# Kernel tuning notes

Measured on AMD Instinct MI355X. Metric: run time of the kernel, lower is better.

## Reference

```python
import jax, jax.numpy as jnp
import numpy as np

N_NODES = 10000
N_EDGES = 160000
MUL = 16          # multiplicity (num_radial channels) per irrep
EMB = 64          # radial_embed_size
HID = 128         # radial_hidden_size
N_PATHS = 5       # (0,0,0),(1,1,0),(0,1,1),(1,0,1),(1,1,1)
W_NUMEL = N_PATHS * MUL * MUL  # 1280


def setup_inputs() -> dict:
    key = jax.random.key(0)
    ks = jax.random.split(key, 9)
    return {
        'edge_index': jax.random.randint(ks[0], (2, N_EDGES), 0, N_NODES),
        'node_feat': jax.random.normal(ks[1], (N_NODES, 4 * MUL), dtype=jnp.float32),
        'edge_feat': jax.random.normal(ks[2], (N_EDGES, 4), dtype=jnp.float32),
        'edge_embed': jax.random.normal(ks[3], (N_EDGES, EMB), dtype=jnp.float32),
        'fc_w1': jax.random.normal(ks[4], (EMB, HID), dtype=jnp.float32),
        'fc_w2': jax.random.normal(ks[5], (HID, HID), dtype=jnp.float32),
        'fc_w3': jax.random.normal(ks[6], (HID, W_NUMEL), dtype=jnp.float32),
        'sc_w0': jax.random.normal(ks[7], (MUL, MUL), dtype=jnp.float32),
        'sc_w1': jax.random.normal(ks[8], (MUL, MUL), dtype=jnp.float32),
    }


def reference(edge_index, node_feat, edge_feat, edge_embed,
              fc_w1, fc_w2, fc_w3, sc_w0, sc_w1):
    """InfGCN GCNLayer: gather src features, fully-connected e3nn-style tensor
    product (irreps '16x0e+16x1o' x SH '1x0e+1x1o' -> '16x0e+16x1o') with
    per-edge weights from a radial MLP, scatter-add into dst, plus o3.Linear
    self-connection. e3nn conventions: FullyConnectedNet normalizes each layer
    by 1/sqrt(fan_in), component irrep_normalization gives w3j factors 1/sqrt(3)
    (1x1->0 dot) and 1/sqrt(2) (1x1->1 cross), element path_normalization gives
    per-path 1/sqrt(mul_in)."""
    E = edge_embed.shape[0]
    N = node_feat.shape[0]
    src, dst = edge_index[0], edge_index[1]

    # radial network (silu on hidden layers, e3nn fan-in normalization)
    h = jax.nn.silu(edge_embed @ (fc_w1 / np.sqrt(EMB)))
    h = jax.nn.silu(h @ (fc_w2 / np.sqrt(HID)))
    w = (h @ (fc_w3 / np.sqrt(HID))).reshape(E, N_PATHS, MUL, MUL)  # [E,P,u,w]

    # gather + split src features into l=0 / l=1 parts
    x = node_feat[src]                       # [E, 64]
    x0 = x[:, :MUL]                          # [E, u]
    x1 = x[:, MUL:].reshape(E, MUL, 3)       # [E, u, 3]
    y0 = edge_feat[:, :1]                    # [E, 1]
    y1 = edge_feat[:, 1:4]                   # [E, 3]

    inv = 1.0 / np.sqrt(MUL)                 # path fan-in normalization
    # l=0 output: paths (0,0,0) and (1,1,0)
    dot = jnp.einsum('eud,ed->eu', x1, y1) / np.sqrt(3.0)
    o0 = (jnp.einsum('euw,eu->ew', w[:, 0], x0 * y0)
          + jnp.einsum('euw,eu->ew', w[:, 1], dot)) * inv     # [E, w]
    # l=1 output: paths (0,1,1), (1,0,1), (1,1,1)
    cross = jnp.cross(x1, y1[:, None, :]) / np.sqrt(2.0)       # [E, u, 3]
    o1 = (jnp.einsum('euw,eu,ed->ewd', w[:, 2], x0, y1)
          + jnp.einsum('euw,eud->ewd', w[:, 3], x1 * y0[:, :, None])
          + jnp.einsum('euw,eud->ewd', w[:, 4], cross)) * inv  # [E, w, 3]

    msg = jnp.concatenate([o0, o1.reshape(E, 3 * MUL)], axis=-1)  # [E, 64]
    out = jax.ops.segment_sum(msg, dst, num_segments=N)            # [N, 64]

    # self-connection: o3.Linear, per-l channel mixing
    s0 = (node_feat[:, :MUL] @ sc_w0) * inv
    s1 = jnp.einsum('nud,uw->nwd', node_feat[:, MUL:].reshape(N, MUL, 3), sc_w1) * inv
    return out + jnp.concatenate([s0, s1.reshape(N, 3 * MUL)], axis=-1)
```

## Files before the change

kernel.cpp:

```cpp
#include <hip/hip_runtime.h>

#define NNODES 10000
#define NEDGES 160000
#define MUL 16
#define EMB 64
#define HID 128

#define RS128 0.08838834764831845f
#define SC3   (0.08838834764831845f * 0.25f)

typedef __attribute__((ext_vector_type(8))) _Float16 half8;
typedef __attribute__((ext_vector_type(4))) _Float16 half4;
typedef __attribute__((ext_vector_type(4))) float f32x4;

__global__ __launch_bounds__(256) void selfconn_kernel(
    const float* __restrict__ node_feat,
    const float* __restrict__ sc_w0,
    const float* __restrict__ sc_w1,
    float* __restrict__ out)
{
    const int tid = threadIdx.x;
    const int nl = tid >> 4;
    const int wp = tid & 15;
    const int n  = blockIdx.x * 16 + nl;

    __shared__ float nf[16][64];
    __shared__ float w0s[16][16];
    __shared__ float w1s[16][16];

    ((float4*)nf)[tid] = ((const float4*)(node_feat + (size_t)blockIdx.x * 16 * 64))[tid];
    if (tid < 64)       ((float4*)w0s)[tid]      = ((const float4*)sc_w0)[tid];
    else if (tid < 128) ((float4*)w1s)[tid - 64] = ((const float4*)sc_w1)[tid - 64];
    __syncthreads();

    float o0 = 0.f, o1x = 0.f, o1y = 0.f, o1z = 0.f;
#pragma unroll
    for (int u = 0; u < 16; ++u) {
        o0 += nf[nl][u] * w0s[u][wp];
        const float wv = w1s[u][wp];
        o1x += nf[nl][16 + u * 3 + 0] * wv;
        o1y += nf[nl][16 + u * 3 + 1] * wv;
        o1z += nf[nl][16 + u * 3 + 2] * wv;
    }
    float* op = out + (size_t)n * 64;
    op[wp]              = o0  * 0.25f;
    op[16 + wp * 3 + 0] = o1x * 0.25f;
    op[16 + wp * 3 + 1] = o1y * 0.25f;
    op[16 + wp * 3 + 2] = o1z * 0.25f;
}

__global__ __launch_bounds__(256) void prep_kernel(
    const float* __restrict__ w1,
    const float* __restrict__ w2,
    const float* __restrict__ w3,
    _Float16* __restrict__ wp)
{
    int idx = blockIdx.x * 256 + threadIdx.x;
    if (idx < 8192) {
        int j = idx & 7, lane = (idx >> 3) & 63, ks = (idx >> 9) & 1, nt = idx >> 10;
        int k = ks * 32 + (lane >> 4) * 8 + j;
        int n = nt * 16 + (lane & 15);
        wp[idx] = (_Float16)(w1[k * HID + n] * 0.125f);
    } else if (idx < 24576) {
        int t = idx - 8192;
        int j = t & 7, lane = (t >> 3) & 63, ks = (t >> 9) & 3, nt = t >> 11;
        int k = ks * 32 + (lane >> 4) * 8 + j;
        int n = nt * 16 + (lane & 15);
        wp[idx] = (_Float16)(w2[k * HID + n] * RS128);
    } else if (idx < 188416) {
        int t = idx - 24576;
        int j = t & 7, lane = (t >> 3) & 63, ks = (t >> 9) & 3, nt = t >> 11;
        int k = ks * 32 + (lane >> 4) * 8 + j;
        int n = nt * 16 + (lane & 15);
        wp[idx] = (_Float16)(w3[k * 1280 + n] * SC3);
    }
}

#define EE_OFF   0
#define H1_OFF   4096
#define H2_OFF   12288
#define SA_OFF   20480
#define SB_OFF   22528
#define SX_OFF   24576
#define SP3_OFF  26624
#define SP4_OFF  32768
#define SY_OFF   38912
#define SEF_OFF  39296
#define SIDX_OFF 39808
#define SMEM_BYTES 40064
#define OPW 65

__global__ __launch_bounds__(256, 4) void edge_mfma_kernel(
    const int*   __restrict__ ei,
    const float* __restrict__ node_feat,
    const float* __restrict__ edge_feat,
    const float* __restrict__ edge_embed,
    const _Float16* __restrict__ wpk,
    float* __restrict__ out)
{
    __shared__ __align__(16) char smem[SMEM_BYTES];

    const int tid = threadIdx.x;
    const int e0  = blockIdx.x * 32;

    int*   sidxp = (int*)(smem + SIDX_OFF);
    float* sEFp  = (float*)(smem + SEF_OFF);

    if (tid < 32)       sidxp[tid] = ei[e0 + tid];
    else if (tid < 64)  sidxp[tid] = ei[NEDGES + e0 + (tid - 32)];
    else if (tid < 192) {
        int t = tid - 64;
        sEFp[t] = edge_feat[e0 * 4 + t];
    }
    __syncthreads();

    float* xg = (float*)(smem + H1_OFF);
    {
        const float4* eesrc = (const float4*)(edge_embed + (size_t)e0 * EMB);
#pragma unroll
        for (int it = 0; it < 2; ++it) {
            int f = tid + it * 256;
            int row = f >> 4, c4 = f & 15;
            float4 v = eesrc[f];
            half4 h = { (_Float16)v.x, (_Float16)v.y, (_Float16)v.z, (_Float16)v.w };
            *(half4*)(smem + EE_OFF + row * 128 + ((c4 * 8) ^ ((row & 7) << 4))) = h;

            int src = sidxp[row];
            float4 nv = ((const float4*)(node_feat + (size_t)src * 64))[c4];
            ((float4*)(xg + row * 64))[c4] = nv;
        }
    }
    __syncthreads();

    {
        float* sAT  = (float*)(smem + SA_OFF);
        float* sBT  = (float*)(smem + SB_OFF);
        float* sXT  = (float*)(smem + SX_OFF);
        float* sP3T = (float*)(smem + SP3_OFF);
        float* sP4T = (float*)(smem + SP4_OFF);
        float* sYT  = (float*)(smem + SY_OFF);
#pragma unroll
        for (int it = 0; it < 2; ++it) {
            int el = (tid >> 4) + it * 16;
            int u  = tid & 15;
            const float* xr = xg + el * 64;
            float x0u = xr[u];
            float xa  = xr[16 + u * 3 + 0];
            float xb  = xr[16 + u * 3 + 1];
            float xc  = xr[16 + u * 3 + 2];
            float y0  = sEFp[el * 4 + 0];
            float y1x = sEFp[el * 4 + 1];
            float y1y = sEFp[el * 4 + 2];
            float y1z = sEFp[el * 4 + 3];
            sXT[u * 32 + el] = x0u;
            sAT[u * 32 + el] = x0u * y0;
            sBT[u * 32 + el] = (xa * y1x + xb * y1y + xc * y1z) * 0.5773502691896258f;
            sP3T[u * 96 + el * 3 + 0] = xa * y0;
            sP3T[u * 96 + el * 3 + 1] = xb * y0;
            sP3T[u * 96 + el * 3 + 2] = xc * y0;
            sP4T[u * 96 + el * 3 + 0] = (xb * y1z - xc * y1y) * 0.7071067811865476f;
            sP4T[u * 96 + el * 3 + 1] = (xc * y1x - xa * y1z) * 0.7071067811865476f;
            sP4T[u * 96 + el * 3 + 2] = (xa * y1y - xb * y1x) * 0.7071067811865476f;
            if (u < 3) sYT[u * 32 + el] = sEFp[el * 4 + 1 + u];
        }
    }
    __syncthreads();

    const int lane  = tid & 63;
    const int w     = tid >> 6;
    const int wm    = w & 1;
    const int wn    = w >> 1;
    const int aswz  = (lane & 7) << 4;
    const int ako2  = (lane >> 4) * 16;
    const int ccol  = lane & 15;
    const int crow00 = (lane >> 4) * 4;

    const half8* w1p8 = (const half8*)wpk;
    const half8* w2p8 = (const half8*)(wpk + 8192);
    const half8* w3p8 = (const half8*)(wpk + 24576);

    {
        const int arow = wm * 16 + (lane & 15);
        half8 a0 = *(const half8*)(smem + EE_OFF + arow * 128 + ((ako2     ) ^ aswz));
        half8 a1 = *(const half8*)(smem + EE_OFF + arow * 128 + ((64 + ako2) ^ aswz));
        const int crow0 = wm * 16 + crow00;
#pragma unroll
        for (int i = 0; i < 4; ++i) {
            int nt = wn * 4 + i;
            f32x4 c = {0.f, 0.f, 0.f, 0.f};
            c = __builtin_amdgcn_mfma_f32_16x16x32_f16(a0, w1p8[(nt * 2 + 0) * 64 + lane], c, 0, 0, 0);
            c = __builtin_amdgcn_mfma_f32_16x16x32_f16(a1, w1p8[(nt * 2 + 1) * 64 + lane], c, 0, 0, 0);
#pragma unroll
            for (int r = 0; r < 4; ++r) {
                int row = crow0 + r;
                int col = nt * 16 + ccol;
                float x = c[r];
                float s = x / (1.f + __expf(-x));
                *(_Float16*)(smem + H1_OFF + row * 256 + ((col * 2) ^ ((row & 7) << 4))) = (_Float16)s;
            }
        }
    }
    __syncthreads();

    {
        const int arow = wm * 16 + (lane & 15);
        half8 a2[4];
#pragma unroll
        for (int ks = 0; ks < 4; ++ks)
            a2[ks] = *(const half8*)(smem + H1_OFF + arow * 256 + ((ks * 64 + ako2) ^ aswz));
        const int crow0 = wm * 16 + crow00;
#pragma unroll
        for (int i = 0; i < 4; ++i) {
            int nt = wn * 4 + i;
            f32x4 c = {0.f, 0.f, 0.f, 0.f};
#pragma unroll
            for (int ks = 0; ks < 4; ++ks)
                c = __builtin_amdgcn_mfma_f32_16x16x32_f16(a2[ks], w2p8[(nt * 4 + ks) * 64 + lane], c, 0, 0, 0);
#pragma unroll
            for (int r = 0; r < 4; ++r) {
                int row = crow0 + r;
                int col = nt * 16 + ccol;
                float x = c[r];
                float s = x / (1.f + __expf(-x));
                *(_Float16*)(smem + H2_OFF + row * 256 + ((col * 2) ^ ((row & 7) << 4))) = (_Float16)s;
            }
        }
    }
    __syncthreads();

    half8 a3[2][4];
#pragma unroll
    for (int m = 0; m < 2; ++m) {
        const int arow = m * 16 + (lane & 15);
#pragma unroll
        for (int ks = 0; ks < 4; ++ks)
            a3[m][ks] = *(const half8*)(smem + H2_OFF + arow * 256 + ((ks * 64 + ako2) ^ aswz));
    }

    float acc0[2][4] = {{0,0,0,0},{0,0,0,0}};
    float s2  [2][4] = {{0,0,0,0},{0,0,0,0}};
    float acc1[2][4][3] = {};

#define MM8(NT, C0, C1) { \
    const half8* bp = w3p8 + (size_t)(NT) * 256 + lane; \
    half8 b0 = bp[0], b1 = bp[64], b2 = bp[128], b3 = bp[192]; \
    C0 = __builtin_amdgcn_mfma_f32_16x16x32_f16(a3[0][0], b0, C0, 0, 0, 0); \
    C1 = __builtin_amdgcn_mfma_f32_16x16x32_f16(a3[1][0], b0, C1, 0, 0, 0); \
    C0 = __builtin_amdgcn_mfma_f32_16x16x32_f16(a3[0][1], b1, C0, 0, 0, 0); \
    C1 = __builtin_amdgcn_mfma_f32_16x16x32_f16(a3[1][1], b1, C1, 0, 0, 0); \
    C0 = __builtin_amdgcn_mfma_f32_16x16x32_f16(a3[0][2], b2, C0, 0, 0, 0); \
    C1 = __builtin_amdgcn_mfma_f32_16x16x32_f16(a3[1][2], b2, C1, 0, 0, 0); \
    C0 = __builtin_amdgcn_mfma_f32_16x16x32_f16(a3[0][3], b3, C0, 0, 0, 0); \
    C1 = __builtin_amdgcn_mfma_f32_16x16x32_f16(a3[1][3], b3, C1, 0, 0, 0); }

#define EPI_T(U, TOFF, ACC) { \
    float4 t0 = *(const float4*)(smem + (TOFF) + (U) * 128 + crow00 * 4); \
    float4 t1 = *(const float4*)(smem + (TOFF) + (U) * 128 + crow00 * 4 + 64); \
    ACC[0][0] += c0[0] * t0.x; ACC[0][1] += c0[1] * t0.y; \
    ACC[0][2] += c0[2] * t0.z; ACC[0][3] += c0[3] * t0.w; \
    ACC[1][0] += c1[0] * t1.x; ACC[1][1] += c1[1] * t1.y; \
    ACC[1][2] += c1[2] * t1.z; ACC[1][3] += c1[3] * t1.w; }

#define EPI_V(U, TOFF) { \
    const char* tb = smem + (TOFF) + (U) * 384 + crow00 * 12; \
    float4 q0 = *(const float4*)(tb);      \
    float4 q1 = *(const float4*)(tb + 16); \
    float4 q2 = *(const float4*)(tb + 32); \
    acc1[0][0][0] += c0[0]*q0.x; acc1[0][0][1] += c0[0]*q0.y; acc1[0][0][2] += c0[0]*q0.z; \
    acc1[0][1][0] += c0[1]*q0.w; acc1[0][1][1] += c0[1]*q1.x; acc1[0][1][2] += c0[1]*q1.y; \
    acc1[0][2][0] += c0[2]*q1.z; acc1[0][2][1] += c0[2]*q1.w; acc1[0][2][2] += c0[2]*q2.x; \
    acc1[0][3][0] += c0[3]*q2.y; acc1[0][3][1] += c0[3]*q2.z; acc1[0][3][2] += c0[3]*q2.w; \
    float4 p0 = *(const float4*)(tb + 192); \
    float4 p1 = *(const float4*)(tb + 208); \
    float4 p2 = *(const float4*)(tb + 224); \
    acc1[1][0][0] += c1[0]*p0.x; acc1[1][0][1] += c1[0]*p0.y; acc1[1][0][2] += c1[0]*p0.z; \
    acc1[1][1][0] += c1[1]*p0.w; acc1[1][1][1] += c1[1]*p1.x; acc1[1][1][2] += c1[1]*p1.y; \
    acc1[1][2][0] += c1[2]*p1.z; acc1[1][2][1] += c1[2]*p1.w; acc1[1][2][2] += c1[2]*p2.x; \
    acc1[1][3][0] += c1[3]*p2.y; acc1[1][3][1] += c1[3]*p2.z; acc1[1][3][2] += c1[3]*p2.w; }

#define TILE_T(NT, U, TOFF, ACC) { \
    f32x4 c0 = {0.f,0.f,0.f,0.f}, c1 = {0.f,0.f,0.f,0.f}; \
    MM8(NT, c0, c1); EPI_T(U, TOFF, ACC); }

#define TILE_V(NT, U, TOFF) { \
    f32x4 c0 = {0.f,0.f,0.f,0.f}, c1 = {0.f,0.f,0.f,0.f}; \
    MM8(NT, c0, c1); EPI_V(U, TOFF); }

    switch (w) {
    case 0:
#pragma unroll 4
        for (int u = 0; u < 16; ++u) TILE_T(u, u, SA_OFF, acc0);
#pragma unroll
        for (int u = 0; u < 4; ++u)  TILE_T(16 + u, u, SB_OFF, acc0);
        break;
    case 1:
#pragma unroll 4
        for (int u = 4; u < 16; ++u) TILE_T(16 + u, u, SB_OFF, acc0);
#pragma unroll 4
        for (int u = 0; u < 8; ++u)  TILE_T(32 + u, u, SX_OFF, s2);
        break;
    case 2:
#pragma unroll 4
        for (int u = 8; u < 16; ++u) TILE_T(32 + u, u, SX_OFF, s2);
#pragma unroll 4
        for (int u = 0; u < 12; ++u) TILE_V(48 + u, u, SP3_OFF);
        break;
    default:
#pragma unroll
        for (int u = 12; u < 16; ++u) TILE_V(48 + u, u, SP3_OFF);
#pragma unroll 4
        for (int u = 0; u < 16; ++u)  TILE_V(64 + u, u, SP4_OFF);
        break;
    }
#undef MM8
#undef EPI_T
#undef EPI_V
#undef TILE_T
#undef TILE_V

#pragma unroll
    for (int m = 0; m < 2; ++m) {
        const char* yb = smem + SY_OFF + crow00 * 4 + m * 64;
        float4 yx = *(const float4*)(yb);
        float4 yy = *(const float4*)(yb + 128);
        float4 yz = *(const float4*)(yb + 256);
        acc1[m][0][0] += s2[m][0] * yx.x; acc1[m][0][1] += s2[m][0] * yy.x; acc1[m][0][2] += s2[m][0] * yz.x;
        acc1[m][1][0] += s2[m][1] * yx.y; acc1[m][1][1] += s2[m][1] * yy.y; acc1[m][1][2] += s2[m][1] * yz.y;
        acc1[m][2][0] += s2[m][2] * yx.z; acc1[m][2][1] += s2[m][2] * yy.z; acc1[m][2][2] += s2[m][2] * yz.z;
        acc1[m][3][0] += s2[m][3] * yx.w; acc1[m][3][1] += s2[m][3] * yy.w; acc1[m][3][2] += s2[m][3] * yz.w;
    }

    __syncthreads();

    {
        float* myop = (float*)smem + w * 32 * OPW;
#pragma unroll
        for (int m = 0; m < 2; ++m)
#pragma unroll
            for (int r = 0; r < 4; ++r) {
                int row = crow00 + m * 16 + r;
                float* rp = myop + row * OPW;
                rp[ccol]                 = acc0[m][r];
                rp[16 + ccol * 3 + 0]    = acc1[m][r][0];
                rp[16 + ccol * 3 + 1]    = acc1[m][r][1];
                rp[16 + ccol * 3 + 2]    = acc1[m][r][2];
            }
    }
    __syncthreads();

    {
        const float* opf = (const float*)smem;
        const int rloc = lane >> 4;
#pragma unroll
        for (int rr = 0; rr < 2; ++rr) {
            int row = w * 8 + rr * 4 + rloc;
            int dst = sidxp[32 + row];
            float* op = out + (size_t)dst * 64;
            float v = opf[0 * 32 * OPW + row * OPW + ccol]
                    + opf[1 * 32 * OPW + row * OPW + ccol]
                    + opf[2 * 32 * OPW + row * OPW + ccol]
                    + opf[3 * 32 * OPW + row * OPW + ccol];
            atomicAdd(op + ccol, v);
#pragma unroll
            for (int d = 0; d < 3; ++d) {
                int c = 16 + ccol * 3 + d;
                float v1 = opf[0 * 32 * OPW + row * OPW + c]
                         + opf[1 * 32 * OPW + row * OPW + c]
                         + opf[2 * 32 * OPW + row * OPW + c]
                         + opf[3 * 32 * OPW + row * OPW + c];
                atomicAdd(op + c, v1);
            }
        }
    }
}

extern "C" void kernel_launch(void* const* d_in, const int* in_sizes, int n_in,
                              void* d_out, int out_size, void* d_ws, size_t ws_size,
                              hipStream_t stream) {
    const int*   ei         = (const int*)  d_in[0];
    const float* node_feat  = (const float*)d_in[1];
    const float* edge_feat  = (const float*)d_in[2];
    const float* edge_embed = (const float*)d_in[3];
    const float* fc_w1      = (const float*)d_in[4];
    const float* fc_w2      = (const float*)d_in[5];
    const float* fc_w3      = (const float*)d_in[6];
    const float* sc_w0      = (const float*)d_in[7];
    const float* sc_w1      = (const float*)d_in[8];
    float* out = (float*)d_out;
    _Float16* wpk = (_Float16*)d_ws;

    prep_kernel<<<736, 256, 0, stream>>>(fc_w1, fc_w2, fc_w3, wpk);
    selfconn_kernel<<<NNODES / 16, 256, 0, stream>>>(node_feat, sc_w0, sc_w1, out);
    edge_mfma_kernel<<<NEDGES / 32, 256, 0, stream>>>(ei, node_feat, edge_feat, edge_embed,
                                                      wpk, out);
}
```

Before: 149.0 us.

## Reuse one LDS buffer for hidden layers, pad operand tiles, fold y-product into staging

```diff
diff --git a/kernel.cpp b/kernel.cpp
--- a/kernel.cpp
+++ b/kernel.cpp
@@ -77,17 +77,15 @@
 }
 
 #define EE_OFF   0
-#define H1_OFF   4096
-#define H2_OFF   12288
-#define SA_OFF   20480
-#define SB_OFF   22528
-#define SX_OFF   24576
-#define SP3_OFF  26624
-#define SP4_OFF  32768
-#define SY_OFF   38912
-#define SEF_OFF  39296
-#define SIDX_OFF 39808
-#define SMEM_BYTES 40064
+#define H_OFF    4096
+#define SA_OFF   12800
+#define SB_OFF   15104
+#define SXY_OFF  17408
+#define SP3_OFF  23808
+#define SP4_OFF  30208
+#define SEF_OFF  36608
+#define SIDX_OFF 37120
+#define SMEM_BYTES 37376
 #define OPW 65
 
 __global__ __launch_bounds__(256, 4) void edge_mfma_kernel(
@@ -114,7 +112,7 @@
     }
     __syncthreads();
 
-    float* xg = (float*)(smem + H1_OFF);
+    float* xg = (float*)(smem + H_OFF);
     {
         const float4* eesrc = (const float4*)(edge_embed + (size_t)e0 * EMB);
 #pragma unroll
@@ -127,42 +125,35 @@
 
             int src = sidxp[row];
             float4 nv = ((const float4*)(node_feat + (size_t)src * 64))[c4];
-            ((float4*)(xg + row * 64))[c4] = nv;
-        }
-    }
-    __syncthreads();
-
-    {
-        float* sAT  = (float*)(smem + SA_OFF);
-        float* sBT  = (float*)(smem + SB_OFF);
-        float* sXT  = (float*)(smem + SX_OFF);
-        float* sP3T = (float*)(smem + SP3_OFF);
-        float* sP4T = (float*)(smem + SP4_OFF);
-        float* sYT  = (float*)(smem + SY_OFF);
-#pragma unroll
-        for (int it = 0; it < 2; ++it) {
-            int el = (tid >> 4) + it * 16;
-            int u  = tid & 15;
-            const float* xr = xg + el * 64;
-            float x0u = xr[u];
-            float xa  = xr[16 + u * 3 + 0];
-            float xb  = xr[16 + u * 3 + 1];
-            float xc  = xr[16 + u * 3 + 2];
-            float y0  = sEFp[el * 4 + 0];
-            float y1x = sEFp[el * 4 + 1];
-            float y1y = sEFp[el * 4 + 2];
-            float y1z = sEFp[el * 4 + 3];
-            sXT[u * 32 + el] = x0u;
-            sAT[u * 32 + el] = x0u * y0;
-            sBT[u * 32 + el] = (xa * y1x + xb * y1y + xc * y1z) * 0.5773502691896258f;
-            sP3T[u * 96 + el * 3 + 0] = xa * y0;
-            sP3T[u * 96 + el * 3 + 1] = xb * y0;
-            sP3T[u * 96 + el * 3 + 2] = xc * y0;
-            sP4T[u * 96 + el * 3 + 0] = (xb * y1z - xc * y1y) * 0.7071067811865476f;
-            sP4T[u * 96 + el * 3 + 1] = (xc * y1x - xa * y1z) * 0.7071067811865476f;
-            sP4T[u * 96 + el * 3 + 2] = (xa * y1y - xb * y1x) * 0.7071067811865476f;
-            if (u < 3) sYT[u * 32 + el] = sEFp[el * 4 + 1 + u];
-        }
+            ((float4*)(xg + row * 68))[c4] = nv;
+        }
+    }
+    __syncthreads();
+
+#pragma unroll
+    for (int it = 0; it < 2; ++it) {
+        int el = (tid >> 4) + it * 16;
+        int u  = tid & 15;
+        const float* xr = xg + el * 68;
+        float x0u = xr[u];
+        float xa  = xr[16 + u * 3 + 0];
+        float xb  = xr[16 + u * 3 + 1];
+        float xc  = xr[16 + u * 3 + 2];
+        float y0  = sEFp[el * 4 + 0];
+        float y1x = sEFp[el * 4 + 1];
+        float y1y = sEFp[el * 4 + 2];
+        float y1z = sEFp[el * 4 + 3];
+        *(float*)(smem + SA_OFF + u * 144 + el * 4) = x0u * y0;
+        *(float*)(smem + SB_OFF + u * 144 + el * 4) =
+            (xa * y1x + xb * y1y + xc * y1z) * 0.5773502691896258f;
+        float* xy = (float*)(smem + SXY_OFF + u * 400 + el * 12);
+        xy[0] = x0u * y1x; xy[1] = x0u * y1y; xy[2] = x0u * y1z;
+        float* p3 = (float*)(smem + SP3_OFF + u * 400 + el * 12);
+        p3[0] = xa * y0; p3[1] = xb * y0; p3[2] = xc * y0;
+        float* p4 = (float*)(smem + SP4_OFF + u * 400 + el * 12);
+        p4[0] = (xb * y1z - xc * y1y) * 0.7071067811865476f;
+        p4[1] = (xc * y1x - xa * y1z) * 0.7071067811865476f;
+        p4[2] = (xa * y1y - xb * y1x) * 0.7071067811865476f;
     }
     __syncthreads();
 
@@ -196,7 +187,7 @@
                 int col = nt * 16 + ccol;
                 float x = c[r];
                 float s = x / (1.f + __expf(-x));
-                *(_Float16*)(smem + H1_OFF + row * 256 + ((col * 2) ^ ((row & 7) << 4))) = (_Float16)s;
+                *(_Float16*)(smem + H_OFF + row * 256 + ((col * 2) ^ ((row & 7) << 4))) = (_Float16)s;
             }
         }
     }
@@ -207,8 +198,9 @@
         half8 a2[4];
 #pragma unroll
         for (int ks = 0; ks < 4; ++ks)
-            a2[ks] = *(const half8*)(smem + H1_OFF + arow * 256 + ((ks * 64 + ako2) ^ aswz));
+            a2[ks] = *(const half8*)(smem + H_OFF + arow * 256 + ((ks * 64 + ako2) ^ aswz));
         const int crow0 = wm * 16 + crow00;
+        f32x4 cs[4];
 #pragma unroll
         for (int i = 0; i < 4; ++i) {
             int nt = wn * 4 + i;
@@ -216,13 +208,19 @@
 #pragma unroll
             for (int ks = 0; ks < 4; ++ks)
                 c = __builtin_amdgcn_mfma_f32_16x16x32_f16(a2[ks], w2p8[(nt * 4 + ks) * 64 + lane], c, 0, 0, 0);
+            cs[i] = c;
+        }
+        __syncthreads();
+#pragma unroll
+        for (int i = 0; i < 4; ++i) {
+            int nt = wn * 4 + i;
 #pragma unroll
             for (int r = 0; r < 4; ++r) {
                 int row = crow0 + r;
                 int col = nt * 16 + ccol;
-                float x = c[r];
+                float x = cs[i][r];
                 float s = x / (1.f + __expf(-x));
-                *(_Float16*)(smem + H2_OFF + row * 256 + ((col * 2) ^ ((row & 7) << 4))) = (_Float16)s;
+                *(_Float16*)(smem + H_OFF + row * 256 + ((col * 2) ^ ((row & 7) << 4))) = (_Float16)s;
             }
         }
     }
@@ -234,11 +232,10 @@
         const int arow = m * 16 + (lane & 15);
 #pragma unroll
         for (int ks = 0; ks < 4; ++ks)
-            a3[m][ks] = *(const half8*)(smem + H2_OFF + arow * 256 + ((ks * 64 + ako2) ^ aswz));
+            a3[m][ks] = *(const half8*)(smem + H_OFF + arow * 256 + ((ks * 64 + ako2) ^ aswz));
     }
 
     float acc0[2][4] = {{0,0,0,0},{0,0,0,0}};
-    float s2  [2][4] = {{0,0,0,0},{0,0,0,0}};
     float acc1[2][4][3] = {};
 
 #define MM8(NT, C0, C1) { \
@@ -253,16 +250,17 @@
     C0 = __builtin_amdgcn_mfma_f32_16x16x32_f16(a3[0][3], b3, C0, 0, 0, 0); \
     C1 = __builtin_amdgcn_mfma_f32_16x16x32_f16(a3[1][3], b3, C1, 0, 0, 0); }
 
-#define EPI_T(U, TOFF, ACC) { \
-    float4 t0 = *(const float4*)(smem + (TOFF) + (U) * 128 + crow00 * 4); \
-    float4 t1 = *(const float4*)(smem + (TOFF) + (U) * 128 + crow00 * 4 + 64); \
-    ACC[0][0] += c0[0] * t0.x; ACC[0][1] += c0[1] * t0.y; \
-    ACC[0][2] += c0[2] * t0.z; ACC[0][3] += c0[3] * t0.w; \
-    ACC[1][0] += c1[0] * t1.x; ACC[1][1] += c1[1] * t1.y; \
-    ACC[1][2] += c1[2] * t1.z; ACC[1][3] += c1[3] * t1.w; }
+#define EPI_T(U, TOFF) { \
+    const char* tb = smem + (TOFF) + (U) * 144 + crow00 * 4; \
+    float4 t0 = *(const float4*)(tb); \
+    float4 t1 = *(const float4*)(tb + 64); \
+    acc0[0][0] += c0[0] * t0.x; acc0[0][1] += c0[1] * t0.y; \
+    acc0[0][2] += c0[2] * t0.z; acc0[0][3] += c0[3] * t0.w; \
+    acc0[1][0] += c1[0] * t1.x; acc0[1][1] += c1[1] * t1.y; \
+    acc0[1][2] += c1[2] * t1.z; acc0[1][3] += c1[3] * t1.w; }
 
 #define EPI_V(U, TOFF) { \
-    const char* tb = smem + (TOFF) + (U) * 384 + crow00 * 12; \
+    const char* tb = smem + (TOFF) + (U) * 400 + crow00 * 12; \
     float4 q0 = *(const float4*)(tb);      \
     float4 q1 = *(const float4*)(tb + 16); \
     float4 q2 = *(const float4*)(tb + 32); \
@@ -278,9 +276,9 @@
     acc1[1][2][0] += c1[2]*p1.z; acc1[1][2][1] += c1[2]*p1.w; acc1[1][2][2] += c1[2]*p2.x; \
     acc1[1][3][0] += c1[3]*p2.y; acc1[1][3][1] += c1[3]*p2.z; acc1[1][3][2] += c1[3]*p2.w; }
 
-#define TILE_T(NT, U, TOFF, ACC) { \
+#define TILE_T(NT, U, TOFF) { \
     f32x4 c0 = {0.f,0.f,0.f,0.f}, c1 = {0.f,0.f,0.f,0.f}; \
-    MM8(NT, c0, c1); EPI_T(U, TOFF, ACC); }
+    MM8(NT, c0, c1); EPI_T(U, TOFF); }
 
 #define TILE_V(NT, U, TOFF) { \
     f32x4 c0 = {0.f,0.f,0.f,0.f}, c1 = {0.f,0.f,0.f,0.f}; \
@@ -289,19 +287,19 @@
     switch (w) {
     case 0:
 #pragma unroll 4
-        for (int u = 0; u < 16; ++u) TILE_T(u, u, SA_OFF, acc0);
-#pragma unroll
-        for (int u = 0; u < 4; ++u)  TILE_T(16 + u, u, SB_OFF, acc0);
+        for (int u = 0; u < 16; ++u) TILE_T(u, u, SA_OFF);
+#pragma unroll
+        for (int u = 0; u < 4; ++u)  TILE_T(16 + u, u, SB_OFF);
         break;
     case 1:
 #pragma unroll 4
-        for (int u = 4; u < 16; ++u) TILE_T(16 + u, u, SB_OFF, acc0);
-#pragma unroll 4
-        for (int u = 0; u < 8; ++u)  TILE_T(32 + u, u, SX_OFF, s2);
+        for (int u = 4; u < 16; ++u) TILE_T(16 + u, u, SB_OFF);
+#pragma unroll 4
+        for (int u = 0; u < 8; ++u)  TILE_V(32 + u, u, SXY_OFF);
         break;
     case 2:
 #pragma unroll 4
-        for (int u = 8; u < 16; ++u) TILE_T(32 + u, u, SX_OFF, s2);
+        for (int u = 8; u < 16; ++u) TILE_V(32 + u, u, SXY_OFF);
 #pragma unroll 4
         for (int u = 0; u < 12; ++u) TILE_V(48 + u, u, SP3_OFF);
         break;
@@ -318,18 +316,6 @@
 #undef TILE_T
 #undef TILE_V
 
-#pragma unroll
-    for (int m = 0; m < 2; ++m) {
-        const char* yb = smem + SY_OFF + crow00 * 4 + m * 64;
-        float4 yx = *(const float4*)(yb);
-        float4 yy = *(const float4*)(yb + 128);
-        float4 yz = *(const float4*)(yb + 256);
-        acc1[m][0][0] += s2[m][0] * yx.x; acc1[m][0][1] += s2[m][0] * yy.x; acc1[m][0][2] += s2[m][0] * yz.x;
-        acc1[m][1][0] += s2[m][1] * yx.y; acc1[m][1][1] += s2[m][1] * yy.y; acc1[m][1][2] += s2[m][1] * yz.y;
-        acc1[m][2][0] += s2[m][2] * yx.z; acc1[m][2][1] += s2[m][2] * yy.z; acc1[m][2][2] += s2[m][2] * yz.z;
-        acc1[m][3][0] += s2[m][3] * yx.w; acc1[m][3][1] += s2[m][3] * yy.w; acc1[m][3][2] += s2[m][3] * yz.w;
-    }
-
     __syncthreads();
 
     {
@@ -340,10 +326,10 @@
             for (int r = 0; r < 4; ++r) {
                 int row = crow00 + m * 16 + r;
                 float* rp = myop + row * OPW;
-                rp[ccol]                 = acc0[m][r];
-                rp[16 + ccol * 3 + 0]    = acc1[m][r][0];
-                rp[16 + ccol * 3 + 1]    = acc1[m][r][1];
-                rp[16 + ccol * 3 + 2]    = acc1[m][r][2];
+                rp[ccol]              = acc0[m][r];
+                rp[16 + ccol * 3 + 0] = acc1[m][r][0];
+                rp[16 + ccol * 3 + 1] = acc1[m][r][1];
+                rp[16 + ccol * 3 + 2] = acc1[m][r][2];
             }
     }
     __syncthreads();
@@ -356,19 +342,15 @@
             int row = w * 8 + rr * 4 + rloc;
             int dst = sidxp[32 + row];
             float* op = out + (size_t)dst * 64;
-            float v = opf[0 * 32 * OPW + row * OPW + ccol]
-                    + opf[1 * 32 * OPW + row * OPW + ccol]
-                    + opf[2 * 32 * OPW + row * OPW + ccol]
-                    + opf[3 * 32 * OPW + row * OPW + ccol];
+            float v = opf[row * OPW + ccol]        + opf[2080 + row * OPW + ccol]
+                    + opf[4160 + row * OPW + ccol] + opf[6240 + row * OPW + ccol];
             atomicAdd(op + ccol, v);
 #pragma unroll
             for (int d = 0; d < 3; ++d) {
-                int c = 16 + ccol * 3 + d;
-                float v1 = opf[0 * 32 * OPW + row * OPW + c]
-                         + opf[1 * 32 * OPW + row * OPW + c]
-                         + opf[2 * 32 * OPW + row * OPW + c]
-                         + opf[3 * 32 * OPW + row * OPW + c];
-                atomicAdd(op + c, v1);
+                int cc = 16 + ccol * 3 + d;
+                float v1 = opf[row * OPW + cc]        + opf[2080 + row * OPW + cc]
+                         + opf[4160 + row * OPW + cc] + opf[6240 + row * OPW + cc];
+                atomicAdd(op + cc, v1);
             }
         }
     }
```

After: 150.4 us. Within noise of the previous version (+0.9%).
